# Optimization experiments

Measured on AMD Instinct MI355X. Metric: run time of the kernel, lower is better.

## Reference

```python
import jax, jax.numpy as jnp
import numpy as np

SUBSTEPS = 2  # fixed RK4 substeps per observation interval (replaces adaptive Tsit5)


def setup_inputs() -> dict:
    key = jax.random.key(0)
    k1, k2, k3, k4, k5 = jax.random.split(key, 5)
    n, d, c, T = 20000, 64, 8, 8
    m, nnz = 5000, 320000
    return {
        "y0": jax.random.normal(k1, (n, d), dtype=jnp.float32),
        "ts": jnp.arange(T, dtype=jnp.float32),
        "controls": jax.random.normal(k2, (T, n, c), dtype=jnp.float32),
        "W": 0.05 * jax.random.normal(k3, (d, d * c), dtype=jnp.float32),
        "b": jnp.zeros((d * c,), dtype=jnp.float32),
        "node_idx": jax.random.randint(k4, (nnz,), 0, n, dtype=jnp.int32),
        "edge_idx": jax.random.randint(k5, (nnz,), 0, m, dtype=jnp.int32),
        "num_edges": m,
    }


def reference(y0, ts, controls, W, b, node_idx, edge_idx, num_edges):
    n, d = y0.shape
    c = controls.shape[-1]
    m = int(num_edges)

    ones = jnp.ones(node_idx.shape[0], dtype=y0.dtype)
    edge_deg = jnp.maximum(jax.ops.segment_sum(ones, edge_idx, num_segments=m), 1.0)
    node_deg = jnp.maximum(jax.ops.segment_sum(ones, node_idx, num_segments=n), 1.0)

    def conv(y):  # HGNN-style two-hop mean aggregation, then linear (n,d)->(n,d*c)
        e = jax.ops.segment_sum(y[node_idx], edge_idx, num_segments=m) / edge_deg[:, None]
        agg = jax.ops.segment_sum(e[edge_idx], node_idx, num_segments=n) / node_deg[:, None]
        return agg @ W + b

    # backward Hermite spline knot derivatives (diffrax backward_hermite_coefficients)
    dt = (ts[1:] - ts[:-1])[:, None, None]            # (T-1,1,1)
    diffs = (controls[1:] - controls[:-1]) / dt        # (T-1,n,c)
    derivs = jnp.concatenate([diffs[:1], diffs], 0)    # (T,n,c)

    def control_deriv(t, seg):  # dX/dt on interval via cubic Hermite basis derivatives
        h = seg["t1"] - seg["t0"]
        s = (t - seg["t0"]) / h
        return (((6 * s * s - 6 * s) / h) * seg["x0"]
                + (3 * s * s - 4 * s + 1) * seg["d0"]
                + ((-6 * s * s + 6 * s) / h) * seg["x1"]
                + (3 * s * s - 2 * s) * seg["d1"])

    def drift(t, y, seg):  # f(y) reshaped (n,d,c), contracted with dX/dt (n,c)
        raw = jnp.tanh(conv(y))
        mat = raw.reshape(n, d, c)
        return jnp.einsum('ndc,nc->nd', mat, control_deriv(t, seg))

    def interval_step(y, seg):
        h = (seg["t1"] - seg["t0"]) / SUBSTEPS
        for k in range(SUBSTEPS):
            t = seg["t0"] + k * h
            k1 = drift(t, y, seg)
            k2 = drift(t + 0.5 * h, y + 0.5 * h * k1, seg)
            k3 = drift(t + 0.5 * h, y + 0.5 * h * k2, seg)
            k4 = drift(t + h, y + h * k3, seg)
            y = y + (h / 6.0) * (k1 + 2 * k2 + 2 * k3 + k4)
        return y, y

    segs = {"t0": ts[:-1], "t1": ts[1:],
            "x0": controls[:-1], "x1": controls[1:],
            "d0": derivs[:-1], "d1": derivs[1:]}
    _, ys_tail = jax.lax.scan(interval_step, y0, segs)
    return jnp.concatenate([y0[None], ys_tail], axis=0)  # (T,n,d)
```

## Files before the change

kernel.cpp:

```cpp
#include <hip/hip_runtime.h>


typedef __attribute__((ext_vector_type(8))) short bfrag8;
typedef __attribute__((ext_vector_type(4))) float f32x4;

__device__ __forceinline__ float bf2f(ushort u) {
  union { uint i; float f; } v; v.i = (uint)u << 16; return v.f;
}
__device__ __forceinline__ ushort f2bf(float f) {
  union { uint i; float f; } v; v.f = f;
  uint r = v.i + 0x7fff + ((v.i >> 16) & 1);
  return (ushort)(r >> 16);
}
__device__ __forceinline__ uint pack2(float lo, float hi) {
  return ((uint)f2bf(hi) << 16) | (uint)f2bf(lo);
}

__global__ __launch_bounds__(256) void k_count(const int* __restrict__ node_idx,
                                               const int* __restrict__ edge_idx,
                                               int* __restrict__ cnt_e,
                                               int* __restrict__ cnt_n, int nnz,
                                               const float* __restrict__ W,
                                               const float* __restrict__ y0,
                                               ushort* __restrict__ Wt,
                                               ushort* __restrict__ y0bf,
                                               int nW, int nY) {
  int j = blockIdx.x * 256 + threadIdx.x;
  if (j < nnz) {
    atomicAdd(&cnt_e[edge_idx[j]], 1);
    atomicAdd(&cnt_n[node_idx[j]], 1);
  }
  int stride = gridDim.x * 256;
  for (int i = j; i < nY; i += stride) y0bf[i] = f2bf(y0[i]);
  for (int i = j; i < nW; i += stride) {
    int k = i >> 9, c = i & 511;
    Wt[c * 64 + k] = f2bf(W[i]);
  }
}

__global__ __launch_bounds__(1024) void k_scan2(const int* __restrict__ cnt_e,
                                                int* __restrict__ off_e,
                                                int* __restrict__ cur_e, int m,
                                                const int* __restrict__ cnt_n,
                                                int* __restrict__ off_n,
                                                int* __restrict__ cur_n, int n) {
  const int* cnt = (blockIdx.x == 0) ? cnt_e : cnt_n;
  int* off = (blockIdx.x == 0) ? off_e : off_n;
  int* cur = (blockIdx.x == 0) ? cur_e : cur_n;
  int len = (blockIdx.x == 0) ? m : n;
  __shared__ int sd[1024];
  __shared__ int s_run;
  if (threadIdx.x == 0) s_run = 0;
  __syncthreads();
  for (int base = 0; base < len; base += 1024) {
    int i = base + threadIdx.x;
    int v = (i < len) ? cnt[i] : 0;
    sd[threadIdx.x] = v;
    __syncthreads();
    for (int ofs = 1; ofs < 1024; ofs <<= 1) {
      int tv = (threadIdx.x >= ofs) ? sd[threadIdx.x - ofs] : 0;
      __syncthreads();
      sd[threadIdx.x] += tv;
      __syncthreads();
    }
    int run = s_run;
    if (i < len) {
      int excl = run + sd[threadIdx.x] - v;
      off[i] = excl;
      cur[i] = excl;
    }
    __syncthreads();
    if (threadIdx.x == 1023) s_run = run + sd[1023];
    __syncthreads();
  }
  if (threadIdx.x == 0) off[len] = s_run;
}

__global__ __launch_bounds__(256) void k_fill(const int* __restrict__ node_idx,
                                              const int* __restrict__ edge_idx,
                                              int* __restrict__ cur_e,
                                              int* __restrict__ cur_n,
                                              int* __restrict__ csr_e,
                                              int* __restrict__ csr_n, int nnz,
                                              const int* __restrict__ cnt_e,
                                              const int* __restrict__ cnt_n,
                                              float* __restrict__ inv_e,
                                              float* __restrict__ inv_n,
                                              int m, int n) {
  int j = blockIdx.x * 256 + threadIdx.x;
  if (j < nnz) {
    int v = node_idx[j], e = edge_idx[j];
    int pe = atomicAdd(&cur_e[e], 1);
    csr_e[pe] = v;
    int pn = atomicAdd(&cur_n[v], 1);
    csr_n[pn] = e;
  }
  if (j < m) inv_e[j] = 1.f / (float)max(cnt_e[j], 1);
  if (j < n) inv_n[j] = 1.f / (float)max(cnt_n[j], 1);
}

__device__ __forceinline__ void seg_gather(const uint* __restrict__ src,
                                           const int* __restrict__ csr,
                                           int p, int pe, int cp,
                                           float& A0, float& A1) {
  float a0 = 0.f, a1 = 0.f, b0 = 0.f, b1 = 0.f;
  for (; p + 14 < pe; p += 16) {
    int r0 = csr[p],      r1 = csr[p + 2],  r2 = csr[p + 4],  r3 = csr[p + 6];
    int r4 = csr[p + 8],  r5 = csr[p + 10], r6 = csr[p + 12], r7 = csr[p + 14];
    uint v0 = src[(size_t)r0 * 32 + cp];
    uint v1 = src[(size_t)r1 * 32 + cp];
    uint v2 = src[(size_t)r2 * 32 + cp];
    uint v3 = src[(size_t)r3 * 32 + cp];
    uint v4 = src[(size_t)r4 * 32 + cp];
    uint v5 = src[(size_t)r5 * 32 + cp];
    uint v6 = src[(size_t)r6 * 32 + cp];
    uint v7 = src[(size_t)r7 * 32 + cp];
    a0 += bf2f((ushort)(v0 & 0xffff)) + bf2f((ushort)(v2 & 0xffff))
        + bf2f((ushort)(v4 & 0xffff)) + bf2f((ushort)(v6 & 0xffff));
    a1 += bf2f((ushort)(v0 >> 16)) + bf2f((ushort)(v2 >> 16))
        + bf2f((ushort)(v4 >> 16)) + bf2f((ushort)(v6 >> 16));
    b0 += bf2f((ushort)(v1 & 0xffff)) + bf2f((ushort)(v3 & 0xffff))
        + bf2f((ushort)(v5 & 0xffff)) + bf2f((ushort)(v7 & 0xffff));
    b1 += bf2f((ushort)(v1 >> 16)) + bf2f((ushort)(v3 >> 16))
        + bf2f((ushort)(v5 >> 16)) + bf2f((ushort)(v7 >> 16));
  }
  if (p + 6 < pe) {
    int r0 = csr[p], r1 = csr[p + 2], r2 = csr[p + 4], r3 = csr[p + 6];
    uint v0 = src[(size_t)r0 * 32 + cp];
    uint v1 = src[(size_t)r1 * 32 + cp];
    uint v2 = src[(size_t)r2 * 32 + cp];
    uint v3 = src[(size_t)r3 * 32 + cp];
    a0 += bf2f((ushort)(v0 & 0xffff)) + bf2f((ushort)(v2 & 0xffff));
    a1 += bf2f((ushort)(v0 >> 16)) + bf2f((ushort)(v2 >> 16));
    b0 += bf2f((ushort)(v1 & 0xffff)) + bf2f((ushort)(v3 & 0xffff));
    b1 += bf2f((ushort)(v1 >> 16)) + bf2f((ushort)(v3 >> 16));
    p += 8;
  }
  if (p + 2 < pe) {
    int r0 = csr[p], r1 = csr[p + 2];
    uint v0 = src[(size_t)r0 * 32 + cp];
    uint v1 = src[(size_t)r1 * 32 + cp];
    a0 += bf2f((ushort)(v0 & 0xffff));
    a1 += bf2f((ushort)(v0 >> 16));
    b0 += bf2f((ushort)(v1 & 0xffff));
    b1 += bf2f((ushort)(v1 >> 16));
    p += 4;
  }
  if (p < pe) {
    uint v0 = src[(size_t)csr[p] * 32 + cp];
    a0 += bf2f((ushort)(v0 & 0xffff));
    a1 += bf2f((ushort)(v0 >> 16));
  }
  A0 = a0 + b0;
  A1 = a1 + b1;
}

__global__ __launch_bounds__(256) void k_seg_mean_bf(const uint* __restrict__ src,
                                                     const int* __restrict__ off,
                                                     const int* __restrict__ csr,
                                                     const float* __restrict__ invdeg,
                                                     uint* __restrict__ dst,
                                                     int nseg) {
  int gid = blockIdx.x * 256 + threadIdx.x;
  int seg = gid >> 6;
  if (seg >= nseg) return;
  int lane = gid & 63;
  int half = lane >> 5;
  int cp = lane & 31;
  float sc = invdeg[seg];
  float a0, a1;
  seg_gather(src, csr, off[seg] + half, off[seg + 1], cp, a0, a1);
  a0 += __shfl_xor(a0, 32);
  a1 += __shfl_xor(a1, 32);
  if (half == 0)
    dst[(size_t)seg * 32 + cp] = pack2(a0 * sc, a1 * sc);
}

__global__ __launch_bounds__(1024, 8) void k_drift_f(
    const uint* __restrict__ e_bf,
    const int* __restrict__ off_n, const int* __restrict__ csr_n,
    const float* __restrict__ invdeg_n,
    const ushort* __restrict__ Wt, const float* __restrict__ bvec,
    const float* __restrict__ controls, const float* __restrict__ ts,
    const float* __restrict__ y_base, float* __restrict__ acc_out,
    uint* __restrict__ ybf,
    int t, int stage, int substep, int n) {
  __shared__ uint aggs[16][36];
  __shared__ float Us[16][8];
  __shared__ float kvs[16][68];

  const int tid = threadIdx.x;
  const int w = tid >> 6;
  const int lane = tid & 63;
  const int half = lane >> 5;
  const int cp = lane & 31;
  const int nodebase = blockIdx.x * 16;

  float t0v = ts[t], t1v = ts[t + 1];
  float h = t1v - t0v;
  float hs = 0.5f * h;
  float soff = (stage == 1) ? 0.f : (stage == 4) ? 1.f : 0.5f;
  float s = ((float)substep + soff) * 0.5f;
  float s2 = s * s;
  float cx0 = (6.f * s2 - 6.f * s) / h;
  float cd0 = 3.f * s2 - 4.f * s + 1.f;
  float cx1 = (-6.f * s2 + 6.f * s) / h;
  float cd1 = 3.f * s2 - 2.f * s;
  float a_m1, a_0, a_p1;
  if (t == 0) {
    a_m1 = 0.f;
    a_0 = cx0 - cd1 / h - cd0 / h;
    a_p1 = cx1 + cd1 / h + cd0 / h;
  } else {
    float hm = t0v - ts[t - 1];
    a_m1 = -cd0 / hm;
    a_0 = cx0 - cd1 / h + cd0 / hm;
    a_p1 = cx1 + cd1 / h;
  }
  int tm1 = (t > 0) ? t - 1 : 0;
  float wk = ((stage == 2 || stage == 3) ? 2.f : 1.f) * hs * (1.f / 6.f);
  float cst = (stage == 3) ? hs : 0.5f * hs;

  if (tid < 128) {
    int nl = tid >> 3, ci = tid & 7;
    size_t bi = (size_t)(nodebase + nl) * 8 + ci;
    float c0 = controls[(size_t)t * n * 8 + bi];
    float cp1 = controls[(size_t)(t + 1) * n * 8 + bi];
    float cm1 = controls[(size_t)tm1 * n * 8 + bi];
    Us[nl][ci] = a_m1 * cm1 + a_0 * c0 + a_p1 * cp1;
  }

  {
    int gnode = nodebase + w;
    float sc = invdeg_n[gnode];
    float a0, a1;
    seg_gather(e_bf, csr_n, off_n[gnode] + half, off_n[gnode + 1], cp, a0, a1);
    a0 += __shfl_xor(a0, 32);
    a1 += __shfl_xor(a1, 32);
    if (half == 0) aggs[w][cp] = pack2(a0 * sc, a1 * sc);
  }
  __syncthreads();

  int arow = lane & 15;
  int kof4 = (lane >> 4) * 4;
  bfrag8 af0 = *reinterpret_cast<const bfrag8*>(&aggs[arow][kof4]);
  bfrag8 af1 = *reinterpret_cast<const bfrag8*>(&aggs[arow][kof4 + 16]);
  int ci = lane & 7, g8 = (lane >> 3) & 1;
  int rbase = (lane >> 4) * 4;
  float u_r[4];
  #pragma unroll
  for (int r = 0; r < 4; ++r) u_r[r] = Us[rbase + r][ci];

  #pragma unroll
  for (int ctl = 0; ctl < 2; ++ctl) {
    int col = w * 32 + ctl * 16 + (lane & 15);
    const ushort* wb = Wt + (size_t)col * 64 + (lane >> 4) * 8;
    bfrag8 b0 = *reinterpret_cast<const bfrag8*>(wb);
    bfrag8 b1 = *reinterpret_cast<const bfrag8*>(wb + 32);
    f32x4 acc = (f32x4){0.f, 0.f, 0.f, 0.f};
    acc = __builtin_amdgcn_mfma_f32_16x16x32_bf16(af0, b0, acc, 0, 0, 0);
    acc = __builtin_amdgcn_mfma_f32_16x16x32_bf16(af1, b1, acc, 0, 0, 0);
    float bb = bvec[col];
    int ddl = w * 4 + ctl * 2 + g8;
    #pragma unroll
    for (int r = 0; r < 4; ++r) {
      float x = acc[r] + bb;
      float th = 1.f - 2.f / (__expf(2.f * x) + 1.f);
      float v = th * u_r[r];
      v += __shfl_xor(v, 1);
      v += __shfl_xor(v, 2);
      v += __shfl_xor(v, 4);
      if (ci == 0) kvs[rbase + r][ddl] = v;
    }
  }
  __syncthreads();

  if (tid < 256) {
    int nl4 = tid >> 4;
    int f0 = (tid & 15) * 4;
    size_t o4 = (size_t)(nodebase + nl4) * 64 + f0;
    float4 kv = *reinterpret_cast<float4*>(&kvs[nl4][f0]);
    float4 ya = *reinterpret_cast<const float4*>(y_base + o4);
    float4 pa = ya;
    if (stage != 1) pa = *reinterpret_cast<const float4*>(acc_out + o4);
    float4 na;
    na.x = pa.x + wk * kv.x; na.y = pa.y + wk * kv.y;
    na.z = pa.z + wk * kv.z; na.w = pa.w + wk * kv.w;
    *reinterpret_cast<float4*>(acc_out + o4) = na;
    float4 sa;
    if (stage < 4) {
      sa.x = ya.x + cst * kv.x; sa.y = ya.y + cst * kv.y;
      sa.z = ya.z + cst * kv.z; sa.w = ya.w + cst * kv.w;
    } else sa = na;
    uint2 pk;
    pk.x = pack2(sa.x, sa.y);
    pk.y = pack2(sa.z, sa.w);
    *reinterpret_cast<uint2*>(ybf + ((size_t)(nodebase + nl4) * 32 + f0 / 2)) = pk;
  }
}

extern "C" void kernel_launch(void* const* d_in, const int* in_sizes, int n_in,
                              void* d_out, int out_size, void* d_ws, size_t ws_size,
                              hipStream_t stream) {
  const float* y0 = (const float*)d_in[0];
  const float* ts = (const float*)d_in[1];
  const float* controls = (const float*)d_in[2];
  const float* W = (const float*)d_in[3];
  const float* bvec = (const float*)d_in[4];
  const int* node_idx = (const int*)d_in[5];
  const int* edge_idx = (const int*)d_in[6];

  const int d = 64;
  const int n = in_sizes[0] / d;
  const int T = in_sizes[1];
  const int nnz = in_sizes[5];
  const int m = 5000;

  char* p = (char*)d_ws;
  auto carve = [&](size_t bytes) {
    char* r = p;
    p += (bytes + 255) & ~(size_t)255;
    return r;
  };
  int* cnt_e = (int*)carve((size_t)m * 4);
  int* cnt_n = (int*)carve((size_t)n * 4);
  int* off_e = (int*)carve((size_t)(m + 1) * 4);
  int* cur_e = (int*)carve((size_t)m * 4);
  int* off_n = (int*)carve((size_t)(n + 1) * 4);
  int* cur_n = (int*)carve((size_t)n * 4);
  int* csr_e = (int*)carve((size_t)nnz * 4);
  int* csr_n = (int*)carve((size_t)nnz * 4);
  float* invdeg_e = (float*)carve((size_t)m * 4);
  float* invdeg_n = (float*)carve((size_t)n * 4);
  ushort* Wt = (ushort*)carve((size_t)512 * 64 * 2);
  ushort* ybf = (ushort*)carve((size_t)n * d * 2);
  ushort* e_bf = (ushort*)carve((size_t)m * d * 2);
  float* y_mid = (float*)carve((size_t)n * d * 4);

  hipMemsetAsync(cnt_e, 0, (size_t)m * 4, stream);
  hipMemsetAsync(cnt_n, 0, (size_t)n * 4, stream);

  k_count<<<(nnz + 255) / 256, 256, 0, stream>>>(node_idx, edge_idx, cnt_e, cnt_n,
                                                 nnz, W, y0, Wt, ybf, 64 * 512, n * d);
  k_scan2<<<2, 1024, 0, stream>>>(cnt_e, off_e, cur_e, m, cnt_n, off_n, cur_n, n);
  k_fill<<<(nnz + 255) / 256, 256, 0, stream>>>(node_idx, edge_idx, cur_e, cur_n,
                                                csr_e, csr_n, nnz, cnt_e, cnt_n,
                                                invdeg_e, invdeg_n, m, n);

  float* out = (float*)d_out;
  hipMemcpyAsync(out, y0, (size_t)n * d * sizeof(float), hipMemcpyDeviceToDevice, stream);

  const int gE = (m * 64 + 255) / 256;
  const int gT = n / 16;

  for (int t = 0; t < T - 1; ++t) {
    float* yout_i = out + (size_t)(t + 1) * n * d;
    for (int sub = 0; sub < 2; ++sub) {
      const float* yb = (sub == 0) ? (out + (size_t)t * n * d) : y_mid;
      float* accp = (sub == 0) ? y_mid : yout_i;
      for (int st = 1; st <= 4; ++st) {
        k_seg_mean_bf<<<gE, 256, 0, stream>>>((const uint*)ybf, off_e, csr_e,
                                              invdeg_e, (uint*)e_bf, m);
        k_drift_f<<<gT, 1024, 0, stream>>>((const uint*)e_bf, off_n, csr_n,
                                           invdeg_n, Wt, bvec, controls, ts,
                                           yb, accp, (uint*)ybf, t, st, sub, n);
      }
    }
  }
}
```

Before: 1.913 ms.

## Fold y0 copy into setup kernel, merge memsets, prefetch weights and state in drift

The y0-to-output copy moves into the k_count conversion loop, and the two count memsets become a single memset over one contiguous buffer. This removes a memcpy and a memset from the launch stream. In the drift kernel, the W fragments, bias, y_base and acc_out loads are hoisted to the start so their latency overlaps the gather phase. The two MFMA column groups are also interleaved, at the cost of more live registers per thread.

```diff
diff --git a/kernel.cpp b/kernel.cpp
--- a/kernel.cpp
+++ b/kernel.cpp
@@ -24,6 +24,7 @@
                                                const float* __restrict__ y0,
                                                ushort* __restrict__ Wt,
                                                ushort* __restrict__ y0bf,
+                                               float* __restrict__ out,
                                                int nW, int nY) {
   int j = blockIdx.x * 256 + threadIdx.x;
   if (j < nnz) {
@@ -31,7 +32,11 @@
     atomicAdd(&cnt_n[node_idx[j]], 1);
   }
   int stride = gridDim.x * 256;
-  for (int i = j; i < nY; i += stride) y0bf[i] = f2bf(y0[i]);
+  for (int i = j; i < nY; i += stride) {
+    float v = y0[i];
+    y0bf[i] = f2bf(v);
+    out[i] = v;
+  }
   for (int i = j; i < nW; i += stride) {
     int k = i >> 9, c = i & 511;
     Wt[c * 64 + k] = f2bf(W[i]);
@@ -196,6 +201,27 @@
   const int cp = lane & 31;
   const int nodebase = blockIdx.x * 16;
 
+  const int colA = w * 32 + (lane & 15);
+  const int colB = colA + 16;
+  const ushort* wbA = Wt + (size_t)colA * 64 + (lane >> 4) * 8;
+  const ushort* wbB = Wt + (size_t)colB * 64 + (lane >> 4) * 8;
+  bfrag8 bA0 = *reinterpret_cast<const bfrag8*>(wbA);
+  bfrag8 bA1 = *reinterpret_cast<const bfrag8*>(wbA + 32);
+  bfrag8 bB0 = *reinterpret_cast<const bfrag8*>(wbB);
+  bfrag8 bB1 = *reinterpret_cast<const bfrag8*>(wbB + 32);
+  float bbA = bvec[colA];
+  float bbB = bvec[colB];
+
+  float4 ya = make_float4(0.f, 0.f, 0.f, 0.f);
+  float4 pa = ya;
+  const int nl4 = tid >> 4;
+  const int f0 = (tid & 15) * 4;
+  const size_t o4 = (size_t)(nodebase + nl4) * 64 + f0;
+  if (tid < 256) {
+    ya = *reinterpret_cast<const float4*>(y_base + o4);
+    pa = (stage == 1) ? ya : *reinterpret_cast<const float4*>(acc_out + o4);
+  }
+
   float t0v = ts[t], t1v = ts[t + 1];
   float h = t1v - t0v;
   float hs = 0.5f * h;
@@ -251,38 +277,37 @@
   #pragma unroll
   for (int r = 0; r < 4; ++r) u_r[r] = Us[rbase + r][ci];
 
-  #pragma unroll
-  for (int ctl = 0; ctl < 2; ++ctl) {
-    int col = w * 32 + ctl * 16 + (lane & 15);
-    const ushort* wb = Wt + (size_t)col * 64 + (lane >> 4) * 8;
-    bfrag8 b0 = *reinterpret_cast<const bfrag8*>(wb);
-    bfrag8 b1 = *reinterpret_cast<const bfrag8*>(wb + 32);
-    f32x4 acc = (f32x4){0.f, 0.f, 0.f, 0.f};
-    acc = __builtin_amdgcn_mfma_f32_16x16x32_bf16(af0, b0, acc, 0, 0, 0);
-    acc = __builtin_amdgcn_mfma_f32_16x16x32_bf16(af1, b1, acc, 0, 0, 0);
-    float bb = bvec[col];
-    int ddl = w * 4 + ctl * 2 + g8;
+  {
+    f32x4 accA = (f32x4){0.f, 0.f, 0.f, 0.f};
+    accA = __builtin_amdgcn_mfma_f32_16x16x32_bf16(af0, bA0, accA, 0, 0, 0);
+    accA = __builtin_amdgcn_mfma_f32_16x16x32_bf16(af1, bA1, accA, 0, 0, 0);
+    f32x4 accB = (f32x4){0.f, 0.f, 0.f, 0.f};
+    accB = __builtin_amdgcn_mfma_f32_16x16x32_bf16(af0, bB0, accB, 0, 0, 0);
+    accB = __builtin_amdgcn_mfma_f32_16x16x32_bf16(af1, bB1, accB, 0, 0, 0);
     #pragma unroll
     for (int r = 0; r < 4; ++r) {
-      float x = acc[r] + bb;
-      float th = 1.f - 2.f / (__expf(2.f * x) + 1.f);
-      float v = th * u_r[r];
-      v += __shfl_xor(v, 1);
-      v += __shfl_xor(v, 2);
-      v += __shfl_xor(v, 4);
-      if (ci == 0) kvs[rbase + r][ddl] = v;
+      float xA = accA[r] + bbA;
+      float thA = 1.f - 2.f / (__expf(2.f * xA) + 1.f);
+      float vA = thA * u_r[r];
+      vA += __shfl_xor(vA, 1);
+      vA += __shfl_xor(vA, 2);
+      vA += __shfl_xor(vA, 4);
+      float xB = accB[r] + bbB;
+      float thB = 1.f - 2.f / (__expf(2.f * xB) + 1.f);
+      float vB = thB * u_r[r];
+      vB += __shfl_xor(vB, 1);
+      vB += __shfl_xor(vB, 2);
+      vB += __shfl_xor(vB, 4);
+      if (ci == 0) {
+        kvs[rbase + r][w * 4 + g8] = vA;
+        kvs[rbase + r][w * 4 + 2 + g8] = vB;
+      }
     }
   }
   __syncthreads();
 
   if (tid < 256) {
-    int nl4 = tid >> 4;
-    int f0 = (tid & 15) * 4;
-    size_t o4 = (size_t)(nodebase + nl4) * 64 + f0;
     float4 kv = *reinterpret_cast<float4*>(&kvs[nl4][f0]);
-    float4 ya = *reinterpret_cast<const float4*>(y_base + o4);
-    float4 pa = ya;
-    if (stage != 1) pa = *reinterpret_cast<const float4*>(acc_out + o4);
     float4 na;
     na.x = pa.x + wk * kv.x; na.y = pa.y + wk * kv.y;
     na.z = pa.z + wk * kv.z; na.w = pa.w + wk * kv.w;
@@ -322,8 +347,9 @@
     p += (bytes + 255) & ~(size_t)255;
     return r;
   };
-  int* cnt_e = (int*)carve((size_t)m * 4);
-  int* cnt_n = (int*)carve((size_t)n * 4);
+  int* cnt = (int*)carve((size_t)(m + n) * 4);
+  int* cnt_e = cnt;
+  int* cnt_n = cnt + m;
   int* off_e = (int*)carve((size_t)(m + 1) * 4);
   int* cur_e = (int*)carve((size_t)m * 4);
   int* off_n = (int*)carve((size_t)(n + 1) * 4);
@@ -337,18 +363,16 @@
   ushort* e_bf = (ushort*)carve((size_t)m * d * 2);
   float* y_mid = (float*)carve((size_t)n * d * 4);
 
-  hipMemsetAsync(cnt_e, 0, (size_t)m * 4, stream);
-  hipMemsetAsync(cnt_n, 0, (size_t)n * 4, stream);
-
+  float* out = (float*)d_out;
+
+  hipMemsetAsync(cnt, 0, (size_t)(m + n) * 4, stream);
   k_count<<<(nnz + 255) / 256, 256, 0, stream>>>(node_idx, edge_idx, cnt_e, cnt_n,
-                                                 nnz, W, y0, Wt, ybf, 64 * 512, n * d);
+                                                 nnz, W, y0, Wt, ybf, out,
+                                                 64 * 512, n * d);
   k_scan2<<<2, 1024, 0, stream>>>(cnt_e, off_e, cur_e, m, cnt_n, off_n, cur_n, n);
   k_fill<<<(nnz + 255) / 256, 256, 0, stream>>>(node_idx, edge_idx, cur_e, cur_n,
                                                 csr_e, csr_n, nnz, cnt_e, cnt_n,
                                                 invdeg_e, invdeg_n, m, n);
-
-  float* out = (float*)d_out;
-  hipMemcpyAsync(out, y0, (size_t)n * d * sizeof(float), hipMemcpyDeviceToDevice, stream);
 
   const int gE = (m * 64 + 255) / 256;
   const int gT = n / 16;
```

After: 2.074 ms. 8.4% more time.

## Split edge gather across two waves, chunk prefix scan, fold y0 copy and memsets

Applied to the files above, without the earlier changes.

The edge-mean kernel now gives each hyperedge two wavefronts (four interleaved lanes-halves) with deeper 8-way unrolled gathers, then combines the partial sums through shared memory. The prefix scan switches from repeated 1024-wide block scans to per-thread serial chunks plus one block scan. The y0 copy to the output is folded into the count kernel, and the two memsets are merged into one. The aim is more memory-level parallelism in the gather, which is launched 64 times, plus fewer setup launches. The cost is a block-wide sync and some idle lanes for low-degree edges.

```diff
diff --git a/kernel.cpp b/kernel.cpp
--- a/kernel.cpp
+++ b/kernel.cpp
@@ -24,6 +24,7 @@
                                                const float* __restrict__ y0,
                                                ushort* __restrict__ Wt,
                                                ushort* __restrict__ y0bf,
+                                               float* __restrict__ out,
                                                int nW, int nY) {
   int j = blockIdx.x * 256 + threadIdx.x;
   if (j < nnz) {
@@ -31,7 +32,11 @@
     atomicAdd(&cnt_n[node_idx[j]], 1);
   }
   int stride = gridDim.x * 256;
-  for (int i = j; i < nY; i += stride) y0bf[i] = f2bf(y0[i]);
+  for (int i = j; i < nY; i += stride) {
+    float v = y0[i];
+    y0bf[i] = f2bf(v);
+    out[i] = v;
+  }
   for (int i = j; i < nW; i += stride) {
     int k = i >> 9, c = i & 511;
     Wt[c * 64 + k] = f2bf(W[i]);
@@ -49,31 +54,28 @@
   int* cur = (blockIdx.x == 0) ? cur_e : cur_n;
   int len = (blockIdx.x == 0) ? m : n;
   __shared__ int sd[1024];
-  __shared__ int s_run;
-  if (threadIdx.x == 0) s_run = 0;
+  int c = (len + 1023) >> 10;
+  int start = threadIdx.x * c;
+  int end = start + c;
+  if (start > len) start = len;
+  if (end > len) end = len;
+  int sum = 0;
+  for (int i = start; i < end; ++i) sum += cnt[i];
+  sd[threadIdx.x] = sum;
   __syncthreads();
-  for (int base = 0; base < len; base += 1024) {
-    int i = base + threadIdx.x;
-    int v = (i < len) ? cnt[i] : 0;
-    sd[threadIdx.x] = v;
+  for (int ofs = 1; ofs < 1024; ofs <<= 1) {
+    int tv = (threadIdx.x >= ofs) ? sd[threadIdx.x - ofs] : 0;
     __syncthreads();
-    for (int ofs = 1; ofs < 1024; ofs <<= 1) {
-      int tv = (threadIdx.x >= ofs) ? sd[threadIdx.x - ofs] : 0;
-      __syncthreads();
-      sd[threadIdx.x] += tv;
-      __syncthreads();
-    }
-    int run = s_run;
-    if (i < len) {
-      int excl = run + sd[threadIdx.x] - v;
-      off[i] = excl;
-      cur[i] = excl;
-    }
+    sd[threadIdx.x] += tv;
     __syncthreads();
-    if (threadIdx.x == 1023) s_run = run + sd[1023];
-    __syncthreads();
-  }
-  if (threadIdx.x == 0) off[len] = s_run;
+  }
+  int run = sd[threadIdx.x] - sum;
+  for (int i = start; i < end; ++i) {
+    off[i] = run;
+    cur[i] = run;
+    run += cnt[i];
+  }
+  if (threadIdx.x == 1023) off[len] = sd[1023];
 }
 
 __global__ __launch_bounds__(256) void k_fill(const int* __restrict__ node_idx,
@@ -161,19 +163,71 @@
                                                      const float* __restrict__ invdeg,
                                                      uint* __restrict__ dst,
                                                      int nseg) {
-  int gid = blockIdx.x * 256 + threadIdx.x;
-  int seg = gid >> 6;
-  if (seg >= nseg) return;
-  int lane = gid & 63;
-  int half = lane >> 5;
-  int cp = lane & 31;
-  float sc = invdeg[seg];
-  float a0, a1;
-  seg_gather(src, csr, off[seg] + half, off[seg + 1], cp, a0, a1);
-  a0 += __shfl_xor(a0, 32);
-  a1 += __shfl_xor(a1, 32);
-  if (half == 0)
-    dst[(size_t)seg * 32 + cp] = pack2(a0 * sc, a1 * sc);
+  __shared__ float part[2][2][2][32];
+  const int tid = threadIdx.x;
+  const int wv = tid >> 6;
+  const int lane = tid & 63;
+  const int half = lane >> 5;
+  const int cp = lane & 31;
+  const int slot = wv >> 1;
+  const int k = wv & 1;
+  const int seg = blockIdx.x * 2 + slot;
+
+  if (seg < nseg) {
+    int p = off[seg] + ((k << 1) | half);
+    int pe = off[seg + 1];
+    float a0 = 0.f, a1 = 0.f, b0 = 0.f, b1 = 0.f;
+    for (; p + 28 < pe; p += 32) {
+      int r0 = csr[p],      r1 = csr[p + 4],  r2 = csr[p + 8],  r3 = csr[p + 12];
+      int r4 = csr[p + 16], r5 = csr[p + 20], r6 = csr[p + 24], r7 = csr[p + 28];
+      uint v0 = src[(size_t)r0 * 32 + cp];
+      uint v1 = src[(size_t)r1 * 32 + cp];
+      uint v2 = src[(size_t)r2 * 32 + cp];
+      uint v3 = src[(size_t)r3 * 32 + cp];
+      uint v4 = src[(size_t)r4 * 32 + cp];
+      uint v5 = src[(size_t)r5 * 32 + cp];
+      uint v6 = src[(size_t)r6 * 32 + cp];
+      uint v7 = src[(size_t)r7 * 32 + cp];
+      a0 += bf2f((ushort)(v0 & 0xffff)) + bf2f((ushort)(v2 & 0xffff))
+          + bf2f((ushort)(v4 & 0xffff)) + bf2f((ushort)(v6 & 0xffff));
+      a1 += bf2f((ushort)(v0 >> 16)) + bf2f((ushort)(v2 >> 16))
+          + bf2f((ushort)(v4 >> 16)) + bf2f((ushort)(v6 >> 16));
+      b0 += bf2f((ushort)(v1 & 0xffff)) + bf2f((ushort)(v3 & 0xffff))
+          + bf2f((ushort)(v5 & 0xffff)) + bf2f((ushort)(v7 & 0xffff));
+      b1 += bf2f((ushort)(v1 >> 16)) + bf2f((ushort)(v3 >> 16))
+          + bf2f((ushort)(v5 >> 16)) + bf2f((ushort)(v7 >> 16));
+    }
+    for (; p + 12 < pe; p += 16) {
+      int r0 = csr[p], r1 = csr[p + 4], r2 = csr[p + 8], r3 = csr[p + 12];
+      uint v0 = src[(size_t)r0 * 32 + cp];
+      uint v1 = src[(size_t)r1 * 32 + cp];
+      uint v2 = src[(size_t)r2 * 32 + cp];
+      uint v3 = src[(size_t)r3 * 32 + cp];
+      a0 += bf2f((ushort)(v0 & 0xffff)) + bf2f((ushort)(v2 & 0xffff));
+      a1 += bf2f((ushort)(v0 >> 16)) + bf2f((ushort)(v2 >> 16));
+      b0 += bf2f((ushort)(v1 & 0xffff)) + bf2f((ushort)(v3 & 0xffff));
+      b1 += bf2f((ushort)(v1 >> 16)) + bf2f((ushort)(v3 >> 16));
+    }
+    for (; p < pe; p += 4) {
+      uint v = src[(size_t)csr[p] * 32 + cp];
+      a0 += bf2f((ushort)(v & 0xffff));
+      a1 += bf2f((ushort)(v >> 16));
+    }
+    a0 += b0; a1 += b1;
+    a0 += __shfl_xor(a0, 32);
+    a1 += __shfl_xor(a1, 32);
+    if (half == 0) {
+      part[slot][k][0][cp] = a0;
+      part[slot][k][1][cp] = a1;
+    }
+  }
+  __syncthreads();
+  if (k == 0 && half == 0 && seg < nseg) {
+    float sc = invdeg[seg];
+    float A0 = part[slot][0][0][cp] + part[slot][1][0][cp];
+    float A1 = part[slot][0][1][cp] + part[slot][1][1][cp];
+    dst[(size_t)seg * 32 + cp] = pack2(A0 * sc, A1 * sc);
+  }
 }
 
 __global__ __launch_bounds__(1024, 8) void k_drift_f(
@@ -322,8 +376,9 @@
     p += (bytes + 255) & ~(size_t)255;
     return r;
   };
-  int* cnt_e = (int*)carve((size_t)m * 4);
-  int* cnt_n = (int*)carve((size_t)n * 4);
+  int* cnt = (int*)carve((size_t)(m + n) * 4);
+  int* cnt_e = cnt;
+  int* cnt_n = cnt + m;
   int* off_e = (int*)carve((size_t)(m + 1) * 4);
   int* cur_e = (int*)carve((size_t)m * 4);
   int* off_n = (int*)carve((size_t)(n + 1) * 4);
@@ -337,20 +392,18 @@
   ushort* e_bf = (ushort*)carve((size_t)m * d * 2);
   float* y_mid = (float*)carve((size_t)n * d * 4);
 
-  hipMemsetAsync(cnt_e, 0, (size_t)m * 4, stream);
-  hipMemsetAsync(cnt_n, 0, (size_t)n * 4, stream);
-
+  float* out = (float*)d_out;
+
+  hipMemsetAsync(cnt, 0, (size_t)(m + n) * 4, stream);
   k_count<<<(nnz + 255) / 256, 256, 0, stream>>>(node_idx, edge_idx, cnt_e, cnt_n,
-                                                 nnz, W, y0, Wt, ybf, 64 * 512, n * d);
+                                                 nnz, W, y0, Wt, ybf, out,
+                                                 64 * 512, n * d);
   k_scan2<<<2, 1024, 0, stream>>>(cnt_e, off_e, cur_e, m, cnt_n, off_n, cur_n, n);
   k_fill<<<(nnz + 255) / 256, 256, 0, stream>>>(node_idx, edge_idx, cur_e, cur_n,
                                                 csr_e, csr_n, nnz, cnt_e, cnt_n,
                                                 invdeg_e, invdeg_n, m, n);
 
-  float* out = (float*)d_out;
-  hipMemcpyAsync(out, y0, (size_t)n * d * sizeof(float), hipMemcpyDeviceToDevice, stream);
-
-  const int gE = (m * 64 + 255) / 256;
+  const int gE = (m + 1) / 2;
   const int gT = n / 16;
 
   for (int t = 0; t < T - 1; ++t) {
```

Result: slower. 2.010 ms (+5.1%).

## Persist drift blocks over tiles, single-pass scan, fuse y0 copy into count

Applied to the files above, without the earlier changes.

The drift kernel now launches a fixed grid of 512 blocks that loop over the 16-node tiles with a grid-stride loop, instead of one block per tile. The two-block prefix scan is replaced by a single pass: each thread sums a contiguous chunk, the block scans those sums, then each thread writes its own offsets. The y0-to-output copy moves into the count kernel, which removes a device memcpy, and the two count memsets become one. The goals are less block scheduling overhead and fewer setup launches. The cost is fewer concurrent waves in the drift kernel, and each block now processes its tiles one after another, so gather latency may be hidden less well.

```diff
diff --git a/kernel.cpp b/kernel.cpp
--- a/kernel.cpp
+++ b/kernel.cpp
@@ -24,6 +24,7 @@
                                                const float* __restrict__ y0,
                                                ushort* __restrict__ Wt,
                                                ushort* __restrict__ y0bf,
+                                               float* __restrict__ out,
                                                int nW, int nY) {
   int j = blockIdx.x * 256 + threadIdx.x;
   if (j < nnz) {
@@ -31,7 +32,11 @@
     atomicAdd(&cnt_n[node_idx[j]], 1);
   }
   int stride = gridDim.x * 256;
-  for (int i = j; i < nY; i += stride) y0bf[i] = f2bf(y0[i]);
+  for (int i = j; i < nY; i += stride) {
+    float v = y0[i];
+    y0bf[i] = f2bf(v);
+    out[i] = v;
+  }
   for (int i = j; i < nW; i += stride) {
     int k = i >> 9, c = i & 511;
     Wt[c * 64 + k] = f2bf(W[i]);
@@ -49,31 +54,28 @@
   int* cur = (blockIdx.x == 0) ? cur_e : cur_n;
   int len = (blockIdx.x == 0) ? m : n;
   __shared__ int sd[1024];
-  __shared__ int s_run;
-  if (threadIdx.x == 0) s_run = 0;
+  int c = (len + 1023) >> 10;
+  int start = threadIdx.x * c;
+  int end = start + c;
+  if (start > len) start = len;
+  if (end > len) end = len;
+  int sum = 0;
+  for (int i = start; i < end; ++i) sum += cnt[i];
+  sd[threadIdx.x] = sum;
   __syncthreads();
-  for (int base = 0; base < len; base += 1024) {
-    int i = base + threadIdx.x;
-    int v = (i < len) ? cnt[i] : 0;
-    sd[threadIdx.x] = v;
+  for (int ofs = 1; ofs < 1024; ofs <<= 1) {
+    int tv = (threadIdx.x >= ofs) ? sd[threadIdx.x - ofs] : 0;
     __syncthreads();
-    for (int ofs = 1; ofs < 1024; ofs <<= 1) {
-      int tv = (threadIdx.x >= ofs) ? sd[threadIdx.x - ofs] : 0;
-      __syncthreads();
-      sd[threadIdx.x] += tv;
-      __syncthreads();
-    }
-    int run = s_run;
-    if (i < len) {
-      int excl = run + sd[threadIdx.x] - v;
-      off[i] = excl;
-      cur[i] = excl;
-    }
+    sd[threadIdx.x] += tv;
     __syncthreads();
-    if (threadIdx.x == 1023) s_run = run + sd[1023];
-    __syncthreads();
-  }
-  if (threadIdx.x == 0) off[len] = s_run;
+  }
+  int run = sd[threadIdx.x] - sum;
+  for (int i = start; i < end; ++i) {
+    off[i] = run;
+    cur[i] = run;
+    run += cnt[i];
+  }
+  if (threadIdx.x == 1023) off[len] = sd[1023];
 }
 
 __global__ __launch_bounds__(256) void k_fill(const int* __restrict__ node_idx,
@@ -184,7 +186,7 @@
     const float* __restrict__ controls, const float* __restrict__ ts,
     const float* __restrict__ y_base, float* __restrict__ acc_out,
     uint* __restrict__ ybf,
-    int t, int stage, int substep, int n) {
+    int t, int stage, int substep, int n, int ntiles) {
   __shared__ uint aggs[16][36];
   __shared__ float Us[16][8];
   __shared__ float kvs[16][68];
@@ -194,7 +196,6 @@
   const int lane = tid & 63;
   const int half = lane >> 5;
   const int cp = lane & 31;
-  const int nodebase = blockIdx.x * 16;
 
   float t0v = ts[t], t1v = ts[t + 1];
   float h = t1v - t0v;
@@ -221,81 +222,85 @@
   float wk = ((stage == 2 || stage == 3) ? 2.f : 1.f) * hs * (1.f / 6.f);
   float cst = (stage == 3) ? hs : 0.5f * hs;
 
-  if (tid < 128) {
-    int nl = tid >> 3, ci = tid & 7;
-    size_t bi = (size_t)(nodebase + nl) * 8 + ci;
-    float c0 = controls[(size_t)t * n * 8 + bi];
-    float cp1 = controls[(size_t)(t + 1) * n * 8 + bi];
-    float cm1 = controls[(size_t)tm1 * n * 8 + bi];
-    Us[nl][ci] = a_m1 * cm1 + a_0 * c0 + a_p1 * cp1;
-  }
-
-  {
-    int gnode = nodebase + w;
-    float sc = invdeg_n[gnode];
-    float a0, a1;
-    seg_gather(e_bf, csr_n, off_n[gnode] + half, off_n[gnode + 1], cp, a0, a1);
-    a0 += __shfl_xor(a0, 32);
-    a1 += __shfl_xor(a1, 32);
-    if (half == 0) aggs[w][cp] = pack2(a0 * sc, a1 * sc);
-  }
-  __syncthreads();
-
-  int arow = lane & 15;
-  int kof4 = (lane >> 4) * 4;
-  bfrag8 af0 = *reinterpret_cast<const bfrag8*>(&aggs[arow][kof4]);
-  bfrag8 af1 = *reinterpret_cast<const bfrag8*>(&aggs[arow][kof4 + 16]);
-  int ci = lane & 7, g8 = (lane >> 3) & 1;
-  int rbase = (lane >> 4) * 4;
-  float u_r[4];
-  #pragma unroll
-  for (int r = 0; r < 4; ++r) u_r[r] = Us[rbase + r][ci];
-
-  #pragma unroll
-  for (int ctl = 0; ctl < 2; ++ctl) {
-    int col = w * 32 + ctl * 16 + (lane & 15);
-    const ushort* wb = Wt + (size_t)col * 64 + (lane >> 4) * 8;
-    bfrag8 b0 = *reinterpret_cast<const bfrag8*>(wb);
-    bfrag8 b1 = *reinterpret_cast<const bfrag8*>(wb + 32);
-    f32x4 acc = (f32x4){0.f, 0.f, 0.f, 0.f};
-    acc = __builtin_amdgcn_mfma_f32_16x16x32_bf16(af0, b0, acc, 0, 0, 0);
-    acc = __builtin_amdgcn_mfma_f32_16x16x32_bf16(af1, b1, acc, 0, 0, 0);
-    float bb = bvec[col];
-    int ddl = w * 4 + ctl * 2 + g8;
+  for (int tile = blockIdx.x; tile < ntiles; tile += gridDim.x) {
+    const int nodebase = tile * 16;
+
+    if (tid < 128) {
+      int nl = tid >> 3, ci = tid & 7;
+      size_t bi = (size_t)(nodebase + nl) * 8 + ci;
+      float c0 = controls[(size_t)t * n * 8 + bi];
+      float cp1 = controls[(size_t)(t + 1) * n * 8 + bi];
+      float cm1 = controls[(size_t)tm1 * n * 8 + bi];
+      Us[nl][ci] = a_m1 * cm1 + a_0 * c0 + a_p1 * cp1;
+    }
+
+    {
+      int gnode = nodebase + w;
+      float sc = invdeg_n[gnode];
+      float a0, a1;
+      seg_gather(e_bf, csr_n, off_n[gnode] + half, off_n[gnode + 1], cp, a0, a1);
+      a0 += __shfl_xor(a0, 32);
+      a1 += __shfl_xor(a1, 32);
+      if (half == 0) aggs[w][cp] = pack2(a0 * sc, a1 * sc);
+    }
+    __syncthreads();
+
+    int arow = lane & 15;
+    int kof4 = (lane >> 4) * 4;
+    bfrag8 af0 = *reinterpret_cast<const bfrag8*>(&aggs[arow][kof4]);
+    bfrag8 af1 = *reinterpret_cast<const bfrag8*>(&aggs[arow][kof4 + 16]);
+    int ci = lane & 7, g8 = (lane >> 3) & 1;
+    int rbase = (lane >> 4) * 4;
+    float u_r[4];
     #pragma unroll
-    for (int r = 0; r < 4; ++r) {
-      float x = acc[r] + bb;
-      float th = 1.f - 2.f / (__expf(2.f * x) + 1.f);
-      float v = th * u_r[r];
-      v += __shfl_xor(v, 1);
-      v += __shfl_xor(v, 2);
-      v += __shfl_xor(v, 4);
-      if (ci == 0) kvs[rbase + r][ddl] = v;
-    }
-  }
-  __syncthreads();
-
-  if (tid < 256) {
-    int nl4 = tid >> 4;
-    int f0 = (tid & 15) * 4;
-    size_t o4 = (size_t)(nodebase + nl4) * 64 + f0;
-    float4 kv = *reinterpret_cast<float4*>(&kvs[nl4][f0]);
-    float4 ya = *reinterpret_cast<const float4*>(y_base + o4);
-    float4 pa = ya;
-    if (stage != 1) pa = *reinterpret_cast<const float4*>(acc_out + o4);
-    float4 na;
-    na.x = pa.x + wk * kv.x; na.y = pa.y + wk * kv.y;
-    na.z = pa.z + wk * kv.z; na.w = pa.w + wk * kv.w;
-    *reinterpret_cast<float4*>(acc_out + o4) = na;
-    float4 sa;
-    if (stage < 4) {
-      sa.x = ya.x + cst * kv.x; sa.y = ya.y + cst * kv.y;
-      sa.z = ya.z + cst * kv.z; sa.w = ya.w + cst * kv.w;
-    } else sa = na;
-    uint2 pk;
-    pk.x = pack2(sa.x, sa.y);
-    pk.y = pack2(sa.z, sa.w);
-    *reinterpret_cast<uint2*>(ybf + ((size_t)(nodebase + nl4) * 32 + f0 / 2)) = pk;
+    for (int r = 0; r < 4; ++r) u_r[r] = Us[rbase + r][ci];
+
+    #pragma unroll
+    for (int ctl = 0; ctl < 2; ++ctl) {
+      int col = w * 32 + ctl * 16 + (lane & 15);
+      const ushort* wb = Wt + (size_t)col * 64 + (lane >> 4) * 8;
+      bfrag8 b0 = *reinterpret_cast<const bfrag8*>(wb);
+      bfrag8 b1 = *reinterpret_cast<const bfrag8*>(wb + 32);
+      f32x4 acc = (f32x4){0.f, 0.f, 0.f, 0.f};
+      acc = __builtin_amdgcn_mfma_f32_16x16x32_bf16(af0, b0, acc, 0, 0, 0);
+      acc = __builtin_amdgcn_mfma_f32_16x16x32_bf16(af1, b1, acc, 0, 0, 0);
+      float bb = bvec[col];
+      int ddl = w * 4 + ctl * 2 + g8;
+      #pragma unroll
+      for (int r = 0; r < 4; ++r) {
+        float x = acc[r] + bb;
+        float th = 1.f - 2.f / (__expf(2.f * x) + 1.f);
+        float v = th * u_r[r];
+        v += __shfl_xor(v, 1);
+        v += __shfl_xor(v, 2);
+        v += __shfl_xor(v, 4);
+        if (ci == 0) kvs[rbase + r][ddl] = v;
+      }
+    }
+    __syncthreads();
+
+    if (tid < 256) {
+      int nl4 = tid >> 4;
+      int f0 = (tid & 15) * 4;
+      size_t o4 = (size_t)(nodebase + nl4) * 64 + f0;
+      float4 kv = *reinterpret_cast<float4*>(&kvs[nl4][f0]);
+      float4 ya = *reinterpret_cast<const float4*>(y_base + o4);
+      float4 pa = ya;
+      if (stage != 1) pa = *reinterpret_cast<const float4*>(acc_out + o4);
+      float4 na;
+      na.x = pa.x + wk * kv.x; na.y = pa.y + wk * kv.y;
+      na.z = pa.z + wk * kv.z; na.w = pa.w + wk * kv.w;
+      *reinterpret_cast<float4*>(acc_out + o4) = na;
+      float4 sa;
+      if (stage < 4) {
+        sa.x = ya.x + cst * kv.x; sa.y = ya.y + cst * kv.y;
+        sa.z = ya.z + cst * kv.z; sa.w = ya.w + cst * kv.w;
+      } else sa = na;
+      uint2 pk;
+      pk.x = pack2(sa.x, sa.y);
+      pk.y = pack2(sa.z, sa.w);
+      *reinterpret_cast<uint2*>(ybf + ((size_t)(nodebase + nl4) * 32 + f0 / 2)) = pk;
+    }
   }
 }
 
@@ -322,8 +327,9 @@
     p += (bytes + 255) & ~(size_t)255;
     return r;
   };
-  int* cnt_e = (int*)carve((size_t)m * 4);
-  int* cnt_n = (int*)carve((size_t)n * 4);
+  int* cnt = (int*)carve((size_t)(m + n) * 4);
+  int* cnt_e = cnt;
+  int* cnt_n = cnt + m;
   int* off_e = (int*)carve((size_t)(m + 1) * 4);
   int* cur_e = (int*)carve((size_t)m * 4);
   int* off_n = (int*)carve((size_t)(n + 1) * 4);
@@ -337,21 +343,20 @@
   ushort* e_bf = (ushort*)carve((size_t)m * d * 2);
   float* y_mid = (float*)carve((size_t)n * d * 4);
 
-  hipMemsetAsync(cnt_e, 0, (size_t)m * 4, stream);
-  hipMemsetAsync(cnt_n, 0, (size_t)n * 4, stream);
-
+  float* out = (float*)d_out;
+
+  hipMemsetAsync(cnt, 0, (size_t)(m + n) * 4, stream);
   k_count<<<(nnz + 255) / 256, 256, 0, stream>>>(node_idx, edge_idx, cnt_e, cnt_n,
-                                                 nnz, W, y0, Wt, ybf, 64 * 512, n * d);
+                                                 nnz, W, y0, Wt, ybf, out,
+                                                 64 * 512, n * d);
   k_scan2<<<2, 1024, 0, stream>>>(cnt_e, off_e, cur_e, m, cnt_n, off_n, cur_n, n);
   k_fill<<<(nnz + 255) / 256, 256, 0, stream>>>(node_idx, edge_idx, cur_e, cur_n,
                                                 csr_e, csr_n, nnz, cnt_e, cnt_n,
                                                 invdeg_e, invdeg_n, m, n);
 
-  float* out = (float*)d_out;
-  hipMemcpyAsync(out, y0, (size_t)n * d * sizeof(float), hipMemcpyDeviceToDevice, stream);
-
   const int gE = (m * 64 + 255) / 256;
-  const int gT = n / 16;
+  const int ntiles = n / 16;
+  const int gT = 512;
 
   for (int t = 0; t < T - 1; ++t) {
     float* yout_i = out + (size_t)(t + 1) * n * d;
@@ -363,7 +368,8 @@
                                               invdeg_e, (uint*)e_bf, m);
         k_drift_f<<<gT, 1024, 0, stream>>>((const uint*)e_bf, off_n, csr_n,
                                            invdeg_n, Wt, bvec, controls, ts,
-                                           yb, accp, (uint*)ybf, t, st, sub, n);
+                                           yb, accp, (uint*)ybf, t, st, sub,
+                                           n, ntiles);
       }
     }
   }
```

New measurement: 1.943 ms. About the same (+1.6%).
